# Kernel optimization log

Hardware: AMD Instinct MI355X
Metric: run time of the kernel (lower is better)

Reference implementation:

```python
import jax, jax.numpy as jnp
import numpy as np

H, W, NC, L = 768, 768, 1, 8
PROJ = L * (L + 1) // 2  # = l*(l-1)/2 + l = 36
LMBDA = 0.1
NU = 0.01
SIGMAP = 1.0 / (3.0 + L)
SIGMAS = 1.0
TAUU = 1.0 / 6.0
N_ITERS = 2  # two primal-dual iterations of run()'s hot loop


def _member_matrix():
    # M[z, K] = 1 iff level z lies in combination K=(k1,k2), k1<=z<=k2.
    # Equivalent to the precomputed k_indices lists in k_indices_for_mu().
    M = np.zeros((L, PROJ), dtype=np.float32)
    K = 0
    for k1 in range(L):
        for k2 in range(k1, L):
            M[k1:k2 + 1, K] = 1.0
            K += 1
    return jnp.asarray(M)

_M = _member_matrix()
_K_OVER_L = jnp.arange(1, L + 1, dtype=jnp.float32) / L  # k/l, k = 1..L


def _fwd_diff(x, axis):
    # torch.cat((torch.diff(x, dim=axis), zeros_like(last slice)), dim=axis)
    pad = [(0, 0)] * x.ndim
    pad[axis] = (0, 1)
    return jnp.pad(jnp.diff(x, axis=axis), pad)


def _div(p, axis):
    # Negative adjoint of _fwd_diff (backward difference with the last
    # slice of p treated as zero): (div p)_j = p_j - p_{j-1}.
    n = p.shape[axis]
    sl = [slice(None)] * p.ndim
    sl[axis] = slice(0, n - 1)
    zpad = [(0, 0)] * p.ndim
    zpad[axis] = (0, 1)
    p_eff = jnp.pad(p[tuple(sl)], zpad)
    spad = [(0, 0)] * p.ndim
    spad[axis] = (1, 0)
    sl2 = [slice(None)] * p.ndim
    sl2[axis] = slice(0, n)
    return p_eff - jnp.pad(p_eff, spad)[tuple(sl2)]


def _parabola(ubar, p1, p2, p3, mu1, mu2, f):
    u1 = _fwd_diff(ubar, 0)
    u2 = _fwd_diff(ubar, 1)
    u3 = _fwd_diff(ubar, 3)
    # level-wise gather-sum over combinations via membership matrix
    mu1sum = jnp.einsum('hwcp,zp->hwcz', mu1, _M)
    mu2sum = jnp.einsum('hwcp,zp->hwcz', mu2, _M)
    u1 = p1 + SIGMAP * (u1 + mu1sum)
    u2 = p2 + SIGMAP * (u2 + mu2sum)
    u3 = p3 + SIGMAP * u3
    quad = LMBDA * (_K_OVER_L - f[..., None]) ** 2      # [h,w,c,L]
    B = 0.25 * (u1 * u1 + u2 * u2) - quad
    mask = u3 < B
    # cubic-root solve projecting onto the parabola
    y = u3 + quad
    norm = jnp.sqrt(u1 * u1 + u2 * u2)
    a = 0.5 * norm                      # 2*0.25*norm
    b = (2.0 / 3.0) * (1.0 - 0.5 * y)   # 2/3*(1 - 2*0.25*y)
    sb = jnp.sqrt(jnp.maximum(-b, 0.0))
    d = jnp.where(b < 0, (a - sb ** 3) * (a + sb ** 3), a * a + b ** 3)
    sd = jnp.sqrt(jnp.maximum(d, 0.0))
    c = jnp.cbrt(a + sd)
    c_safe = jnp.where(c == 0, 1.0, c)
    sb3 = jnp.where(sb > 0, sb ** 3, 1.0)
    cosarg = jnp.clip(a / sb3, -1.0, 1.0)
    v_neg = 2.0 * sb * jnp.cos(jnp.arccos(cosarg) / 3.0)
    v = jnp.where((d >= 0) & (c == 0), 0.0,
                  jnp.where(d < 0, v_neg, c - b / c_safe))
    norm_safe = jnp.where(norm == 0, 1.0, norm)
    scale = (v / 0.5) / norm_safe       # v / (2*0.25) / norm
    p1n = jnp.where(mask, jnp.where(norm == 0, 0.0, scale * u1), u1)
    p2n = jnp.where(mask, jnp.where(norm == 0, 0.0, scale * u2), u2)
    p3n = jnp.where(mask, 0.25 * (p1n * p1n + p2n * p2n) - quad, u3)
    return p1n, p2n, p3n


def _l2projection(s1, s2, mubar1, mubar2):
    m1 = s1 - SIGMAS * mubar1
    m2 = s2 - SIGMAS * mubar2
    norm = jnp.sqrt(m1 * m1 + m2 * m2)
    mask = norm > NU
    ns = jnp.where(mask, norm, 1.0)
    return jnp.where(mask, m1 * NU / ns, m1), jnp.where(mask, m2 * NU / ns, m2)


def _mu(mu1, mu2, s1, s2, p1, p2):
    tau = 1.0 / (2.0 + PROJ / 4.0)
    # t[K] = sum of p over levels k1..k2 for combination K (same membership M)
    t1 = jnp.einsum('hwcz,zp->hwcp', p1, _M)
    t2 = jnp.einsum('hwcz,zp->hwcp', p2, _M)
    mu1n = mu1 + tau * (s1 - t1)
    mu2n = mu2 + tau * (s2 - t2)
    return mu1n, mu2n, 2.0 * mu1n - mu1, 2.0 * mu2n - mu2


def _clipping(u, p1, p2, p3):
    div = _div(p1, 0) + _div(p2, 1) + _div(p3, 3)
    un = jnp.clip(u + TAUU * div, 0.0, 1.0)
    return un, 2.0 * un - u


def setup_inputs() -> dict:
    key = jax.random.key(0)
    ks = jax.random.split(key, 12)
    lvl = (H, W, NC, L)
    prj = (H, W, NC, PROJ)
    return {
        'u': jax.random.uniform(ks[0], lvl, jnp.float32),
        'ubar': jax.random.uniform(ks[1], lvl, jnp.float32),
        'p1': jax.random.normal(ks[2], lvl, jnp.float32),
        'p2': jax.random.normal(ks[3], lvl, jnp.float32),
        'p3': jax.random.normal(ks[4], lvl, jnp.float32),
        's1': jax.random.normal(ks[5], prj, jnp.float32),
        's2': jax.random.normal(ks[6], prj, jnp.float32),
        'mu1': jax.random.normal(ks[7], prj, jnp.float32),
        'mu2': jax.random.normal(ks[8], prj, jnp.float32),
        'mubar1': jax.random.normal(ks[9], prj, jnp.float32),
        'mubar2': jax.random.normal(ks[10], prj, jnp.float32),
        'f': jax.random.uniform(ks[11], (H, W, NC), jnp.float32),
    }


def reference(u, ubar, p1, p2, p3, s1, s2, mu1, mu2, mubar1, mubar2, f):
    for _ in range(N_ITERS):
        p1, p2, p3 = _parabola(ubar, p1, p2, p3, mu1, mu2, f)
        s1, s2 = _l2projection(s1, s2, mubar1, mubar2)
        mu1, mu2, mubar1, mubar2 = _mu(mu1, mu2, s1, s2, p1, p2)
        u, ubar = _clipping(u, p1, p2, p3)
    return u
```

## Files before the change

### kernel.cpp

```cpp
#include <hip/hip_runtime.h>
#include <math.h>

#define HH   768
#define WW   768
#define LL   8
#define NPIX (HH*WW)
#define NLVL (NPIX*LL)
#define BLK  128
#define REC  37

#define SIGMAP (1.0f/11.0f)
#define TAUMU  (1.0f/11.0f)
#define TAUU   (1.0f/6.0f)
#define LMBDA  0.1f
#define NUC    0.01f

__device__ __forceinline__ float4 ld4(const float* p){ return *reinterpret_cast<const float4*>(p); }
__device__ __forceinline__ void  st4(float* p, float4 v){ *reinterpret_cast<float4*>(p) = v; }

__device__ __forceinline__ void ld8(float* d, const float* s){
  float4 a = ld4(s), b = ld4(s+4);
  d[0]=a.x; d[1]=a.y; d[2]=a.z; d[3]=a.w;
  d[4]=b.x; d[5]=b.y; d[6]=b.z; d[7]=b.w;
}
__device__ __forceinline__ void st8(float* d, const float* s){
  st4(d,   make_float4(s[0],s[1],s[2],s[3]));
  st4(d+4, make_float4(s[4],s[5],s[6],s[7]));
}

__device__ __forceinline__ void parabola1(float u1, float u2, float u3, float quad,
                                          float& p1n, float& p2n, float& p3n)
{
  float nn = u1*u1 + u2*u2;
  float Bv = 0.25f*nn - quad;
  if (u3 < Bv) {
    float y    = u3 + quad;
    float norm = sqrtf(nn);
    float a    = 0.5f*norm;
    float b    = (2.0f/3.0f)*(1.0f - 0.5f*y);
    float sb   = sqrtf(fmaxf(-b, 0.0f));
    float sb3  = sb*sb*sb;
    float d    = (b < 0.0f) ? (a - sb3)*(a + sb3) : (a*a + b*b*b);
    float v;
    if (d < 0.0f) {
      float sb3s = (sb > 0.0f) ? sb3 : 1.0f;
      float ca   = fminf(fmaxf(a/sb3s, -1.0f), 1.0f);
      v = 2.0f*sb*cosf(acosf(ca)*(1.0f/3.0f));
    } else {
      float sd = sqrtf(d);
      float c  = cbrtf(a + sd);
      v = (c == 0.0f) ? 0.0f : (c - b/c);
    }
    float nsafe = (norm == 0.0f) ? 1.0f : norm;
    float scale = (v + v)/nsafe;
    p1n = (norm == 0.0f) ? 0.0f : scale*u1;
    p2n = (norm == 0.0f) ? 0.0f : scale*u2;
    p3n = 0.25f*(p1n*p1n + p2n*p2n) - quad;
  } else {
    p1n = u1; p2n = u2; p3n = u3;
  }
}

__device__ __forceinline__ void stage1(const float* __restrict__ g, float* __restrict__ lds, int tid)
{
  #pragma unroll
  for (int j = 0; j < 9; ++j) {
    int g4 = (tid + BLK*j) * 4;
    float4 v = ld4(g + g4);
    int pl  = g4 / 36;
    int off = g4 - pl*36;
    float* d = lds + pl*REC + off;
    d[0]=v.x; d[1]=v.y; d[2]=v.z; d[3]=v.w;
  }
}

__device__ __forceinline__ void stage_diff(const float* __restrict__ ga, const float* __restrict__ gb,
                                           float* __restrict__ lds, int tid)
{
  #pragma unroll
  for (int j = 0; j < 9; ++j) {
    int g4 = (tid + BLK*j) * 4;
    float4 a = ld4(ga + g4);
    float4 b = ld4(gb + g4);
    int pl  = g4 / 36;
    int off = g4 - pl*36;
    float* d = lds + pl*REC + off;
    d[0]=a.x-b.x; d[1]=a.y-b.y; d[2]=a.z-b.z; d[3]=a.w-b.w;
  }
}

__global__ __launch_bounds__(BLK) void k_iter1(
  const float* __restrict__ ubar, const float* __restrict__ p1,
  const float* __restrict__ p2,   const float* __restrict__ p3,
  const float* __restrict__ s1,   const float* __restrict__ s2,
  const float* __restrict__ mu1,  const float* __restrict__ mu2,
  const float* __restrict__ mb1,  const float* __restrict__ mb2,
  const float* __restrict__ f,
  float* __restrict__ op1, float* __restrict__ op2, float* __restrict__ op3,
  float* __restrict__ oms1, float* __restrict__ oms2)
{
  __shared__ float sA[BLK*REC];
  __shared__ float sB[BLK*REC];

  const int tid  = threadIdx.x;
  const int blk0 = blockIdx.x * BLK;
  const int p    = blk0 + tid;
  const int w  = p % WW;
  const int h  = p / WW;
  const int pr = (w < WW-1) ? p+1  : p;
  const int pd = (h < HH-1) ? p+WW : p;

  stage1(mu1 + (size_t)blk0*36, sA, tid);
  stage1(mu2 + (size_t)blk0*36, sB, tid);
  __syncthreads();

  const float* rA = sA + tid*REC;
  const float* rB = sB + tid*REC;
  float ms1[8], ms2[8];
  #pragma unroll
  for (int z=0; z<8; ++z){ ms1[z]=0.f; ms2[z]=0.f; }
  {
    int K = 0;
    #pragma unroll
    for (int k1=0; k1<8; ++k1) {
      #pragma unroll
      for (int k2=k1; k2<8; ++k2) {
        float v1 = rA[K], v2 = rB[K];
        #pragma unroll
        for (int z=k1; z<=k2; ++z){ ms1[z]+=v1; ms2[z]+=v2; }
        ++K;
      }
    }
  }

  float ub[8], ubr[8], ubd[8];
  ld8(ub,  ubar + (size_t)p *8);
  ld8(ubr, ubar + (size_t)pr*8);
  ld8(ubd, ubar + (size_t)pd*8);
  float p1v[8], p2v[8], p3v[8];
  ld8(p1v, p1 + (size_t)p*8);
  ld8(p2v, p2 + (size_t)p*8);
  ld8(p3v, p3 + (size_t)p*8);
  const float fv = f[p];

  float pn1[8], pn2[8], pn3[8];
  #pragma unroll
  for (int z=0; z<8; ++z) {
    float du1 = ubd[z]-ub[z];
    float du2 = ubr[z]-ub[z];
    float du3 = (z<7) ? (ub[z+1]-ub[z]) : 0.f;
    float u1 = p1v[z] + SIGMAP*(du1 + ms1[z]);
    float u2 = p2v[z] + SIGMAP*(du2 + ms2[z]);
    float u3 = p3v[z] + SIGMAP*du3;
    float t  = (float)(z+1)*0.125f - fv;
    float quad = LMBDA*t*t;
    parabola1(u1,u2,u3,quad, pn1[z],pn2[z],pn3[z]);
  }
  st8(op1 + (size_t)p*8, pn1);
  st8(op2 + (size_t)p*8, pn2);
  st8(op3 + (size_t)p*8, pn3);

  float pre1[9], pre2[9];
  pre1[0]=0.f; pre2[0]=0.f;
  #pragma unroll
  for (int z=0; z<8; ++z){ pre1[z+1]=pre1[z]+pn1[z]; pre2[z+1]=pre2[z]+pn2[z]; }

  __syncthreads();
  stage_diff(s1 + (size_t)blk0*36, mb1 + (size_t)blk0*36, sA, tid);
  stage_diff(s2 + (size_t)blk0*36, mb2 + (size_t)blk0*36, sB, tid);
  __syncthreads();

  float A1[8], A2[8];
  #pragma unroll
  for (int z=0; z<8; ++z){ A1[z]=0.f; A2[z]=0.f; }
  {
    int K = 0;
    #pragma unroll
    for (int k1=0; k1<8; ++k1) {
      #pragma unroll
      for (int k2=k1; k2<8; ++k2) {
        float m1 = rA[K], m2 = rB[K];
        float nrm = sqrtf(m1*m1 + m2*m2);
        float s1n, s2n;
        if (nrm > NUC) { float r = NUC/nrm; s1n = m1*r; s2n = m2*r; }
        else           { s1n = m1; s2n = m2; }
        float d1 = s1n - (pre1[k2+1]-pre1[k1]);
        float d2 = s2n - (pre2[k2+1]-pre2[k1]);
        #pragma unroll
        for (int z=k1; z<=k2; ++z){ A1[z]+=d1; A2[z]+=d2; }
        ++K;
      }
    }
  }
  float nms1[8], nms2[8];
  #pragma unroll
  for (int z=0; z<8; ++z){ nms1[z] = ms1[z] + TAUMU*A1[z]; nms2[z] = ms2[z] + TAUMU*A2[z]; }
  st8(oms1 + (size_t)p*8, nms1);
  st8(oms2 + (size_t)p*8, nms2);
}

__global__ __launch_bounds__(256) void k_parab2(
  const float* __restrict__ ubar,
  float* __restrict__ p1, float* __restrict__ p2, float* __restrict__ p3,
  const float* __restrict__ ms1g, const float* __restrict__ ms2g,
  const float* __restrict__ f)
{
  const int p = blockIdx.x*blockDim.x + threadIdx.x;
  if (p >= NPIX) return;
  const int w  = p % WW;
  const int h  = p / WW;
  const int pr = (w < WW-1) ? p+1  : p;
  const int pd = (h < HH-1) ? p+WW : p;

  float ub[8], ubr[8], ubd[8];
  ld8(ub,  ubar + (size_t)p *8);
  ld8(ubr, ubar + (size_t)pr*8);
  ld8(ubd, ubar + (size_t)pd*8);
  float p1v[8], p2v[8], p3v[8];
  ld8(p1v, p1 + (size_t)p*8);
  ld8(p2v, p2 + (size_t)p*8);
  ld8(p3v, p3 + (size_t)p*8);
  float ms1[8], ms2[8];
  ld8(ms1, ms1g + (size_t)p*8);
  ld8(ms2, ms2g + (size_t)p*8);
  const float fv = f[p];

  float pn1[8], pn2[8], pn3[8];
  #pragma unroll
  for (int z=0; z<8; ++z) {
    float du1 = ubd[z]-ub[z];
    float du2 = ubr[z]-ub[z];
    float du3 = (z<7) ? (ub[z+1]-ub[z]) : 0.f;
    float u1 = p1v[z] + SIGMAP*(du1 + ms1[z]);
    float u2 = p2v[z] + SIGMAP*(du2 + ms2[z]);
    float u3 = p3v[z] + SIGMAP*du3;
    float t  = (float)(z+1)*0.125f - fv;
    float quad = LMBDA*t*t;
    parabola1(u1,u2,u3,quad, pn1[z],pn2[z],pn3[z]);
  }
  st8(p1 + (size_t)p*8, pn1);
  st8(p2 + (size_t)p*8, pn2);
  st8(p3 + (size_t)p*8, pn3);
}

__global__ __launch_bounds__(256) void k_clip(
  const float* __restrict__ uin,
  const float* __restrict__ p1, const float* __restrict__ p2,
  const float* __restrict__ p3,
  float* __restrict__ uout, float* __restrict__ ubarout)
{
  const int p = blockIdx.x*blockDim.x + threadIdx.x;
  if (p >= NPIX) return;
  const int w  = p % WW;
  const int h  = p / WW;
  const int pu = (h > 0) ? p-WW : p;
  const int pl = (w > 0) ? p-1  : p;

  float uv[8], a1[8], a1u[8], a2[8], a2l[8], a3[8];
  ld8(uv,  uin + (size_t)p *8);
  ld8(a1,  p1  + (size_t)p *8);
  ld8(a1u, p1  + (size_t)pu*8);
  ld8(a2,  p2  + (size_t)p *8);
  ld8(a2l, p2  + (size_t)pl*8);
  ld8(a3,  p3  + (size_t)p *8);

  const float fh1 = (h < HH-1) ? 1.f : 0.f;
  const float fh0 = (h > 0)    ? 1.f : 0.f;
  const float fw1 = (w < WW-1) ? 1.f : 0.f;
  const float fw0 = (w > 0)    ? 1.f : 0.f;

  float un[8], ubn[8];
  #pragma unroll
  for (int z=0; z<8; ++z) {
    float d1 = fh1*a1[z] - fh0*a1u[z];
    float d2 = fw1*a2[z] - fw0*a2l[z];
    float d3 = ((z<7) ? a3[z] : 0.f) - ((z>0) ? a3[z-1] : 0.f);
    float x  = uv[z] + TAUU*(d1+d2+d3);
    x = fminf(fmaxf(x, 0.f), 1.f);
    un[z]  = x;
    ubn[z] = 2.f*x - uv[z];
  }
  st8(uout + (size_t)p*8, un);
  if (ubarout) st8(ubarout + (size_t)p*8, ubn);
}

extern "C" void kernel_launch(void* const* d_in, const int* in_sizes, int n_in,
                              void* d_out, int out_size, void* d_ws, size_t ws_size,
                              hipStream_t stream)
{
  const float* u    = (const float*)d_in[0];
  const float* ubar = (const float*)d_in[1];
  const float* p1   = (const float*)d_in[2];
  const float* p2   = (const float*)d_in[3];
  const float* p3   = (const float*)d_in[4];
  const float* s1   = (const float*)d_in[5];
  const float* s2   = (const float*)d_in[6];
  const float* mu1  = (const float*)d_in[7];
  const float* mu2  = (const float*)d_in[8];
  const float* mb1  = (const float*)d_in[9];
  const float* mb2  = (const float*)d_in[10];
  const float* f    = (const float*)d_in[11];

  float* ws   = (float*)d_ws;
  float* wp1  = ws;
  float* wp2  = ws + 1*(size_t)NLVL;
  float* wp3  = ws + 2*(size_t)NLVL;
  float* wms1 = ws + 3*(size_t)NLVL;
  float* wms2 = ws + 4*(size_t)NLVL;
  float* wub  = ws + 5*(size_t)NLVL;
  float* uo   = (float*)d_out;

  k_iter1 <<<dim3(NPIX/BLK), dim3(BLK), 0, stream>>>(
      ubar,p1,p2,p3,s1,s2,mu1,mu2,mb1,mb2,f, wp1,wp2,wp3,wms1,wms2);
  k_clip  <<<dim3(NPIX/256), dim3(256), 0, stream>>>(u, wp1,wp2,wp3, uo, wub);
  k_parab2<<<dim3(NPIX/256), dim3(256), 0, stream>>>(wub, wp1,wp2,wp3, wms1,wms2, f);
  k_clip  <<<dim3(NPIX/256), dim3(256), 0, stream>>>(uo, wp1,wp2,wp3, uo, nullptr);
}
```

Baseline: 592.7 us.

## Split each pixel's eight levels across two threads in the fused first-iteration kernel

The fused first-iteration kernel now runs 256 threads per 128-pixel block, with each pixel's 8 levels split into two halves of 4 handled by separate threads. Each thread scans only the combinations that touch its half, and the two halves exchange their new p1/p2 values through LDS to build the prefix sums. The intent is more parallelism and lower per-thread register pressure, which should raise occupancy for this compute- and register-heavy kernel. In exchange it adds extra barriers and LDS traffic, and some combinations are normalised twice because both halves need them.

Result: no change. 591.6 us (-0.2%).

```diff
diff --git a/kernel.cpp b/kernel.cpp
--- a/kernel.cpp
+++ b/kernel.cpp
@@ -7,6 +7,7 @@
 #define NPIX (HH*WW)
 #define NLVL (NPIX*LL)
 #define BLK  128
+#define THR  256
 #define REC  37
 
 #define SIGMAP (1.0f/11.0f)
@@ -61,25 +62,33 @@
   }
 }
 
-__device__ __forceinline__ void stage1(const float* __restrict__ g, float* __restrict__ lds, int tid)
-{
-  #pragma unroll
-  for (int j = 0; j < 9; ++j) {
-    int g4 = (tid + BLK*j) * 4;
+__device__ __forceinline__ void stage1_256(const float* __restrict__ g, float* __restrict__ lds, int tid)
+{
+  #pragma unroll
+  for (int j = 0; j < 4; ++j) {
+    int g4 = (tid + THR*j) * 4;
     float4 v = ld4(g + g4);
     int pl  = g4 / 36;
     int off = g4 - pl*36;
     float* d = lds + pl*REC + off;
     d[0]=v.x; d[1]=v.y; d[2]=v.z; d[3]=v.w;
   }
-}
-
-__device__ __forceinline__ void stage_diff(const float* __restrict__ ga, const float* __restrict__ gb,
-                                           float* __restrict__ lds, int tid)
-{
-  #pragma unroll
-  for (int j = 0; j < 9; ++j) {
-    int g4 = (tid + BLK*j) * 4;
+  if (tid < 128) {
+    int g4 = (tid + 1024) * 4;
+    float4 v = ld4(g + g4);
+    int pl  = g4 / 36;
+    int off = g4 - pl*36;
+    float* d = lds + pl*REC + off;
+    d[0]=v.x; d[1]=v.y; d[2]=v.z; d[3]=v.w;
+  }
+}
+
+__device__ __forceinline__ void stage_diff_256(const float* __restrict__ ga, const float* __restrict__ gb,
+                                               float* __restrict__ lds, int tid)
+{
+  #pragma unroll
+  for (int j = 0; j < 4; ++j) {
+    int g4 = (tid + THR*j) * 4;
     float4 a = ld4(ga + g4);
     float4 b = ld4(gb + g4);
     int pl  = g4 / 36;
@@ -87,9 +96,67 @@
     float* d = lds + pl*REC + off;
     d[0]=a.x-b.x; d[1]=a.y-b.y; d[2]=a.z-b.z; d[3]=a.w-b.w;
   }
-}
-
-__global__ __launch_bounds__(BLK) void k_iter1(
+  if (tid < 128) {
+    int g4 = (tid + 1024) * 4;
+    float4 a = ld4(ga + g4);
+    float4 b = ld4(gb + g4);
+    int pl  = g4 / 36;
+    int off = g4 - pl*36;
+    float* d = lds + pl*REC + off;
+    d[0]=a.x-b.x; d[1]=a.y-b.y; d[2]=a.z-b.z; d[3]=a.w-b.w;
+  }
+}
+
+template<int ZB>
+__device__ __forceinline__ void memb_scan(const float* __restrict__ rA, const float* __restrict__ rB,
+                                          float (&ms1)[4], float (&ms2)[4])
+{
+  int K = 0;
+  #pragma unroll
+  for (int k1 = 0; k1 < 8; ++k1) {
+    #pragma unroll
+    for (int k2 = k1; k2 < 8; ++k2) {
+      if (k2 >= ZB && k1 < ZB + 4) {
+        float v1 = rA[K], v2 = rB[K];
+        #pragma unroll
+        for (int z = (k1 > ZB ? k1 : ZB); z <= (k2 < ZB+3 ? k2 : ZB+3); ++z) {
+          ms1[z-ZB] += v1; ms2[z-ZB] += v2;
+        }
+      }
+      ++K;
+    }
+  }
+}
+
+template<int ZB>
+__device__ __forceinline__ void proj_scan(const float* __restrict__ rA, const float* __restrict__ rB,
+                                          const float (&pre1)[9], const float (&pre2)[9],
+                                          float (&A1)[4], float (&A2)[4])
+{
+  int K = 0;
+  #pragma unroll
+  for (int k1 = 0; k1 < 8; ++k1) {
+    #pragma unroll
+    for (int k2 = k1; k2 < 8; ++k2) {
+      if (k2 >= ZB && k1 < ZB + 4) {
+        float m1 = rA[K], m2 = rB[K];
+        float nrm = sqrtf(m1*m1 + m2*m2);
+        float s1n, s2n;
+        if (nrm > NUC) { float r = NUC/nrm; s1n = m1*r; s2n = m2*r; }
+        else           { s1n = m1; s2n = m2; }
+        float d1 = s1n - (pre1[k2+1] - pre1[k1]);
+        float d2 = s2n - (pre2[k2+1] - pre2[k1]);
+        #pragma unroll
+        for (int z = (k1 > ZB ? k1 : ZB); z <= (k2 < ZB+3 ? k2 : ZB+3); ++z) {
+          A1[z-ZB] += d1; A2[z-ZB] += d2;
+        }
+      }
+      ++K;
+    }
+  }
+}
+
+__global__ __launch_bounds__(THR, 4) void k_iter1(
   const float* __restrict__ ubar, const float* __restrict__ p1,
   const float* __restrict__ p2,   const float* __restrict__ p3,
   const float* __restrict__ s1,   const float* __restrict__ s2,
@@ -103,100 +170,92 @@
   __shared__ float sB[BLK*REC];
 
   const int tid  = threadIdx.x;
+  const int lpx  = tid & 127;
+  const int hi   = tid >> 7;
+  const int zb   = hi * 4;
   const int blk0 = blockIdx.x * BLK;
-  const int p    = blk0 + tid;
+  const int p    = blk0 + lpx;
   const int w  = p % WW;
   const int h  = p / WW;
   const int pr = (w < WW-1) ? p+1  : p;
   const int pd = (h < HH-1) ? p+WW : p;
 
-  stage1(mu1 + (size_t)blk0*36, sA, tid);
-  stage1(mu2 + (size_t)blk0*36, sB, tid);
-  __syncthreads();
-
-  const float* rA = sA + tid*REC;
-  const float* rB = sB + tid*REC;
-  float ms1[8], ms2[8];
-  #pragma unroll
-  for (int z=0; z<8; ++z){ ms1[z]=0.f; ms2[z]=0.f; }
-  {
-    int K = 0;
-    #pragma unroll
-    for (int k1=0; k1<8; ++k1) {
-      #pragma unroll
-      for (int k2=k1; k2<8; ++k2) {
-        float v1 = rA[K], v2 = rB[K];
-        #pragma unroll
-        for (int z=k1; z<=k2; ++z){ ms1[z]+=v1; ms2[z]+=v2; }
-        ++K;
-      }
-    }
-  }
-
-  float ub[8], ubr[8], ubd[8];
-  ld8(ub,  ubar + (size_t)p *8);
-  ld8(ubr, ubar + (size_t)pr*8);
-  ld8(ubd, ubar + (size_t)pd*8);
-  float p1v[8], p2v[8], p3v[8];
-  ld8(p1v, p1 + (size_t)p*8);
-  ld8(p2v, p2 + (size_t)p*8);
-  ld8(p3v, p3 + (size_t)p*8);
+  stage1_256(mu1 + (size_t)blk0*36, sA, tid);
+  stage1_256(mu2 + (size_t)blk0*36, sB, tid);
+  __syncthreads();
+
+  const float* rA = sA + lpx*REC;
+  const float* rB = sB + lpx*REC;
+  float ms1[4] = {0.f,0.f,0.f,0.f}, ms2[4] = {0.f,0.f,0.f,0.f};
+  if (hi) memb_scan<4>(rA, rB, ms1, ms2);
+  else    memb_scan<0>(rA, rB, ms1, ms2);
+
+  float4 ubq  = ld4(ubar + (size_t)p *8 + zb);
+  float  ubx  = hi ? 0.f : ubar[(size_t)p*8 + 4];
+  float4 ubrq = ld4(ubar + (size_t)pr*8 + zb);
+  float4 ubdq = ld4(ubar + (size_t)pd*8 + zb);
+  float4 p1q  = ld4(p1 + (size_t)p*8 + zb);
+  float4 p2q  = ld4(p2 + (size_t)p*8 + zb);
+  float4 p3q  = ld4(p3 + (size_t)p*8 + zb);
   const float fv = f[p];
 
-  float pn1[8], pn2[8], pn3[8];
-  #pragma unroll
-  for (int z=0; z<8; ++z) {
-    float du1 = ubd[z]-ub[z];
-    float du2 = ubr[z]-ub[z];
-    float du3 = (z<7) ? (ub[z+1]-ub[z]) : 0.f;
-    float u1 = p1v[z] + SIGMAP*(du1 + ms1[z]);
-    float u2 = p2v[z] + SIGMAP*(du2 + ms2[z]);
-    float u3 = p3v[z] + SIGMAP*du3;
+  float ubv[5]  = {ubq.x, ubq.y, ubq.z, ubq.w, ubx};
+  float ubrv[4] = {ubrq.x, ubrq.y, ubrq.z, ubrq.w};
+  float ubdv[4] = {ubdq.x, ubdq.y, ubdq.z, ubdq.w};
+  float p1v[4]  = {p1q.x, p1q.y, p1q.z, p1q.w};
+  float p2v[4]  = {p2q.x, p2q.y, p2q.z, p2q.w};
+  float p3v[4]  = {p3q.x, p3q.y, p3q.z, p3q.w};
+
+  float pn1[4], pn2[4], pn3[4];
+  #pragma unroll
+  for (int i = 0; i < 4; ++i) {
+    int z = zb + i;
+    float du1 = ubdv[i] - ubv[i];
+    float du2 = ubrv[i] - ubv[i];
+    float du3 = (z < 7) ? (ubv[i+1] - ubv[i]) : 0.f;
+    float u1 = p1v[i] + SIGMAP*(du1 + ms1[i]);
+    float u2 = p2v[i] + SIGMAP*(du2 + ms2[i]);
+    float u3 = p3v[i] + SIGMAP*du3;
     float t  = (float)(z+1)*0.125f - fv;
     float quad = LMBDA*t*t;
-    parabola1(u1,u2,u3,quad, pn1[z],pn2[z],pn3[z]);
-  }
-  st8(op1 + (size_t)p*8, pn1);
-  st8(op2 + (size_t)p*8, pn2);
-  st8(op3 + (size_t)p*8, pn3);
-
+    parabola1(u1,u2,u3,quad, pn1[i],pn2[i],pn3[i]);
+  }
+  st4(op1 + (size_t)p*8 + zb, make_float4(pn1[0],pn1[1],pn1[2],pn1[3]));
+  st4(op2 + (size_t)p*8 + zb, make_float4(pn2[0],pn2[1],pn2[2],pn2[3]));
+  st4(op3 + (size_t)p*8 + zb, make_float4(pn3[0],pn3[1],pn3[2],pn3[3]));
+
+  __syncthreads();
+  float* ex1 = sA;
+  float* ex2 = sA + 8*BLK;
+  #pragma unroll
+  for (int i = 0; i < 4; ++i) {
+    ex1[(zb+i)*BLK + lpx] = pn1[i];
+    ex2[(zb+i)*BLK + lpx] = pn2[i];
+  }
+  __syncthreads();
   float pre1[9], pre2[9];
-  pre1[0]=0.f; pre2[0]=0.f;
-  #pragma unroll
-  for (int z=0; z<8; ++z){ pre1[z+1]=pre1[z]+pn1[z]; pre2[z+1]=pre2[z]+pn2[z]; }
-
-  __syncthreads();
-  stage_diff(s1 + (size_t)blk0*36, mb1 + (size_t)blk0*36, sA, tid);
-  stage_diff(s2 + (size_t)blk0*36, mb2 + (size_t)blk0*36, sB, tid);
-  __syncthreads();
-
-  float A1[8], A2[8];
-  #pragma unroll
-  for (int z=0; z<8; ++z){ A1[z]=0.f; A2[z]=0.f; }
-  {
-    int K = 0;
-    #pragma unroll
-    for (int k1=0; k1<8; ++k1) {
-      #pragma unroll
-      for (int k2=k1; k2<8; ++k2) {
-        float m1 = rA[K], m2 = rB[K];
-        float nrm = sqrtf(m1*m1 + m2*m2);
-        float s1n, s2n;
-        if (nrm > NUC) { float r = NUC/nrm; s1n = m1*r; s2n = m2*r; }
-        else           { s1n = m1; s2n = m2; }
-        float d1 = s1n - (pre1[k2+1]-pre1[k1]);
-        float d2 = s2n - (pre2[k2+1]-pre2[k1]);
-        #pragma unroll
-        for (int z=k1; z<=k2; ++z){ A1[z]+=d1; A2[z]+=d2; }
-        ++K;
-      }
-    }
-  }
-  float nms1[8], nms2[8];
-  #pragma unroll
-  for (int z=0; z<8; ++z){ nms1[z] = ms1[z] + TAUMU*A1[z]; nms2[z] = ms2[z] + TAUMU*A2[z]; }
-  st8(oms1 + (size_t)p*8, nms1);
-  st8(oms2 + (size_t)p*8, nms2);
+  pre1[0] = 0.f; pre2[0] = 0.f;
+  #pragma unroll
+  for (int z = 0; z < 8; ++z) {
+    pre1[z+1] = pre1[z] + ex1[z*BLK + lpx];
+    pre2[z+1] = pre2[z] + ex2[z*BLK + lpx];
+  }
+
+  __syncthreads();
+  stage_diff_256(s1 + (size_t)blk0*36, mb1 + (size_t)blk0*36, sA, tid);
+  stage_diff_256(s2 + (size_t)blk0*36, mb2 + (size_t)blk0*36, sB, tid);
+  __syncthreads();
+
+  float A1[4] = {0.f,0.f,0.f,0.f}, A2[4] = {0.f,0.f,0.f,0.f};
+  if (hi) proj_scan<4>(rA, rB, pre1, pre2, A1, A2);
+  else    proj_scan<0>(rA, rB, pre1, pre2, A1, A2);
+
+  st4(oms1 + (size_t)p*8 + zb,
+      make_float4(ms1[0] + TAUMU*A1[0], ms1[1] + TAUMU*A1[1],
+                  ms1[2] + TAUMU*A1[2], ms1[3] + TAUMU*A1[3]));
+  st4(oms2 + (size_t)p*8 + zb,
+      make_float4(ms2[0] + TAUMU*A2[0], ms2[1] + TAUMU*A2[1],
+                  ms2[2] + TAUMU*A2[2], ms2[3] + TAUMU*A2[3]));
 }
 
 __global__ __launch_bounds__(256) void k_parab2(
@@ -310,7 +369,7 @@
   float* wub  = ws + 5*(size_t)NLVL;
   float* uo   = (float*)d_out;
 
-  k_iter1 <<<dim3(NPIX/BLK), dim3(BLK), 0, stream>>>(
+  k_iter1 <<<dim3(NPIX/BLK), dim3(THR), 0, stream>>>(
       ubar,p1,p2,p3,s1,s2,mu1,mu2,mb1,mb2,f, wp1,wp2,wp3,wms1,wms2);
   k_clip  <<<dim3(NPIX/256), dim3(256), 0, stream>>>(u, wp1,wp2,wp3, uo, wub);
   k_parab2<<<dim3(NPIX/256), dim3(256), 0, stream>>>(wub, wp1,wp2,wp3, wms1,wms2, f);
```
